# Kernel tuning notes

Hardware: AMD Instinct MI355X
Metric: run time of the kernel (lower is better)

Reference implementation:

```python
import jax, jax.numpy as jnp
import numpy as np

B, T, V = 4, 2048, 2048
D = 256   # state_dim
R = 512   # inner_dim
EPS = float(jnp.finfo(jnp.float32).eps)  # F.rms_norm default eps = dtype eps


def rms_norm(x):
    return x * jax.lax.rsqrt(jnp.mean(x * x, axis=-1, keepdims=True) + EPS)


def setup_inputs() -> dict:
    key = jax.random.key(0)
    ks = jax.random.split(key, 9)
    std = 0.02
    return {
        "x": jax.random.normal(ks[0], (B, T, V), dtype=jnp.float32),
        "Wq": jax.random.normal(ks[1], (D, V), dtype=jnp.float32) * std,
        "Wk": jax.random.normal(ks[2], (D, V), dtype=jnp.float32) * std,
        "Wv": jax.random.normal(ks[3], (D, V), dtype=jnp.float32) * std,
        "Wo": jax.random.normal(ks[4], (V, D), dtype=jnp.float32) * std,
        "decay_logit": jnp.float32(3.0),
        "q_out_scale": jnp.float32(0.1),
        "Wdown": jax.random.normal(ks[5], (R, V), dtype=jnp.float32) * std,
        "Wup": jax.random.normal(ks[6], (V, R), dtype=jnp.float32) * std,
        "t_bias": jnp.zeros((R,), dtype=jnp.float32),
        "t_out_scale": jnp.float32(0.1),
        "q_scale": jnp.ones((1,), dtype=jnp.float32),
        "t_scale": jnp.ones((1,), dtype=jnp.float32),
    }


def qtable(x, Wq, Wk, Wv, Wo, decay_logit, out_scale):
    # x: (B,T,V)
    q = jnp.einsum('btv,dv->btd', x, Wq)
    k = jnp.einsum('btv,dv->btd', x, Wk)
    v = jnp.einsum('btv,dv->btd', x, Wv)
    scores = jnp.einsum('btd,bsd->bts', q, k)  # (B,T,T)
    decay = jax.nn.sigmoid(decay_logit)
    pos = jnp.arange(T)
    diff = pos[None, :] - pos[:, None]  # diff[t,s] = s - t ... matches torch (unsqueeze(0)-unsqueeze(1))
    causal = (diff > 0).astype(jnp.float32)
    weights = decay ** jnp.clip(diff.astype(jnp.float32) - 1.0, 0.0, None) * causal
    scores = scores * weights[None, :, :]
    retrieved = jnp.einsum('bts,bsd->btd', scores, v)
    return jnp.einsum('btd,vd->btv', retrieved, Wo) * out_scale


def transform(x, Wdown, Wup, bias, out_scale):
    h = jnp.einsum('btv,rv->btr', x, Wdown) + bias
    h = jax.nn.gelu(h, approximate=False)
    return jnp.einsum('btr,vr->btv', h, Wup) * out_scale


def reference(x, Wq, Wk, Wv, Wo, decay_logit, q_out_scale,
              Wdown, Wup, t_bias, t_out_scale, q_scale, t_scale):
    x = x + q_scale * qtable(rms_norm(x), Wq, Wk, Wv, Wo, decay_logit, q_out_scale)
    x = x + t_scale * transform(rms_norm(x), Wdown, Wup, t_bias, t_out_scale)
    return x
```

## Files before the change

kernel.cpp:

```cpp
#include <hip/hip_runtime.h>
#include <cmath>

typedef _Float16 f16;
typedef _Float16 f16x8 __attribute__((ext_vector_type(8)));
typedef _Float16 f16x4 __attribute__((ext_vector_type(4)));
typedef float f32x4 __attribute__((ext_vector_type(4)));

#define MFMA16(a, b, c) __builtin_amdgcn_mfma_f32_16x16x32_f16(a, b, c, 0, 0, 0)

static constexpr int Bsz = 4;
static constexpr int T = 2048;
static constexpr int V = 2048;
static constexpr int D = 256;
static constexpr int R = 512;
static constexpr int M = Bsz * T;

__device__ __forceinline__ void load_lds16(const f16* g, f16* l) {
    __builtin_amdgcn_global_load_lds(
        (const __attribute__((address_space(1))) unsigned int*)(unsigned long long)g,
        (__attribute__((address_space(3))) unsigned int*)(unsigned int)(unsigned long long)l,
        16, 0, 0);
}

__global__ __launch_bounds__(256) void conv_all(const float* __restrict__ s0,
                                                const float* __restrict__ s1,
                                                const float* __restrict__ s2,
                                                const float* __restrict__ s3,
                                                const float* __restrict__ s4,
                                                const float* __restrict__ s5,
                                                f16* __restrict__ dst) {
    int idx = (blockIdx.x * 256 + threadIdx.x) * 4;
    if (idx >= 4194304) return;
    const float* src; int off;
    if      (idx <  524288) { src = s0; off = idx; }
    else if (idx < 1048576) { src = s1; off = idx - 524288; }
    else if (idx < 1572864) { src = s2; off = idx - 1048576; }
    else if (idx < 2097152) { src = s3; off = idx - 1572864; }
    else if (idx < 3145728) { src = s4; off = idx - 2097152; }
    else                    { src = s5; off = idx - 3145728; }
    float4 v = *(const float4*)&src[off];
    f16x4 o;
    o[0] = (f16)v.x; o[1] = (f16)v.y; o[2] = (f16)v.z; o[3] = (f16)v.w;
    *(f16x4*)&dst[idx] = o;
}

__global__ __launch_bounds__(256) void rmsnorm_kernel(const float* __restrict__ x,
                                                      f16* __restrict__ out) {
    int row = blockIdx.x;
    const float* xr = x + (size_t)row * V;
    int tid = threadIdx.x;
    float4 v0 = ((const float4*)xr)[tid];
    float4 v1 = ((const float4*)xr)[tid + 256];
    float ss = v0.x * v0.x + v0.y * v0.y + v0.z * v0.z + v0.w * v0.w
             + v1.x * v1.x + v1.y * v1.y + v1.z * v1.z + v1.w * v1.w;
    #pragma unroll
    for (int o = 32; o > 0; o >>= 1) ss += __shfl_xor(ss, o);
    __shared__ float wsum[4];
    if ((tid & 63) == 0) wsum[tid >> 6] = ss;
    __syncthreads();
    float tot = wsum[0] + wsum[1] + wsum[2] + wsum[3];
    float s = rsqrtf(tot / (float)V + 1.1920929e-07f);
    f16* orow = out + (size_t)row * V;
    f16x4 o0, o1;
    o0[0] = (f16)(v0.x * s); o0[1] = (f16)(v0.y * s);
    o0[2] = (f16)(v0.z * s); o0[3] = (f16)(v0.w * s);
    o1[0] = (f16)(v1.x * s); o1[1] = (f16)(v1.y * s);
    o1[2] = (f16)(v1.z * s); o1[3] = (f16)(v1.w * s);
    *(f16x4*)&orow[tid * 4] = o0;
    *(f16x4*)&orow[1024 + tid * 4] = o1;
}

__global__ __launch_bounds__(256) void rmsnorm_f16(const f16* __restrict__ x,
                                                   f16* __restrict__ out) {
    int row = blockIdx.x;
    int tid = threadIdx.x;
    const f16* xr = x + (size_t)row * V;
    f16x8 v = *(const f16x8*)&xr[tid * 8];
    float f[8];
    float ss = 0.f;
    #pragma unroll
    for (int j = 0; j < 8; j++) { f[j] = (float)v[j]; ss += f[j] * f[j]; }
    #pragma unroll
    for (int o = 32; o > 0; o >>= 1) ss += __shfl_xor(ss, o);
    __shared__ float wsum[4];
    if ((tid & 63) == 0) wsum[tid >> 6] = ss;
    __syncthreads();
    float tot = wsum[0] + wsum[1] + wsum[2] + wsum[3];
    float s = rsqrtf(tot / (float)V + 1.1920929e-07f);
    f16x8 o;
    #pragma unroll
    for (int j = 0; j < 8; j++) o[j] = (f16)(f[j] * s);
    *(f16x8*)&out[(size_t)row * V + tid * 8] = o;
}

struct GemmEpi {
    const float* residf;
    const f16* residh;
    float* outf;
    f16* outh;
    f16* out_q; f16* out_k; f16* out_vT;
    f16* out_h;
    const float* bias;
    const float* sA; const float* sB;
};

template <int MODE>
__global__ __launch_bounds__(256) void gemm_nt(const f16* __restrict__ A,
                                               const f16* __restrict__ Bm,
                                               int K, GemmEpi e) {
    __shared__ f16 Asl[2][128 * 32];
    __shared__ f16 Bsl[2][128 * 32];
    int tid = threadIdx.x;
    int lane = tid & 63, wv = tid >> 6;
    int wm = wv >> 1, wn = wv & 1;
    int quad = lane >> 4, l16 = lane & 15;
    int m0 = blockIdx.x * 128, n0 = blockIdx.y * 128;
    f32x4 acc[4][4] = {};

    int srow = lane >> 2;
    int scg = (lane & 3) ^ ((lane >> 3) & 3);
    const f16* Ag0 = &A[(size_t)(m0 + 16 * wv + srow) * K + scg * 8];
    const f16* Ag1 = &A[(size_t)(m0 + 16 * (wv + 4) + srow) * K + scg * 8];
    const f16* Bg0 = &Bm[(size_t)(n0 + 16 * wv + srow) * K + scg * 8];
    const f16* Bg1 = &Bm[(size_t)(n0 + 16 * (wv + 4) + srow) * K + scg * 8];
    int lo0 = (16 * wv) * 32, lo1 = (16 * (wv + 4)) * 32;

    int fs = quad ^ ((l16 >> 1) & 3);
    int niter = K >> 5;

    load_lds16(Ag0, &Asl[0][lo0]);
    load_lds16(Ag1, &Asl[0][lo1]);
    load_lds16(Bg0, &Bsl[0][lo0]);
    load_lds16(Bg1, &Bsl[0][lo1]);

    for (int i = 0; i < niter; i++) {
        int cur = i & 1;
        __builtin_amdgcn_s_barrier();
        if (i + 1 < niter) {
            int k0 = (i + 1) << 5;
            int nb = cur ^ 1;
            load_lds16(Ag0 + k0, &Asl[nb][lo0]);
            load_lds16(Ag1 + k0, &Asl[nb][lo1]);
            load_lds16(Bg0 + k0, &Bsl[nb][lo0]);
            load_lds16(Bg1 + k0, &Bsl[nb][lo1]);
            asm volatile("s_waitcnt vmcnt(4)" ::: "memory");
        } else {
            asm volatile("s_waitcnt vmcnt(0)" ::: "memory");
        }
        __builtin_amdgcn_s_barrier();
        f16x8 af[4], bf[4];
        #pragma unroll
        for (int j = 0; j < 4; j++)
            af[j] = *(const f16x8*)&Asl[cur][(64 * wm + 16 * j + l16) * 32 + fs * 8];
        #pragma unroll
        for (int j = 0; j < 4; j++)
            bf[j] = *(const f16x8*)&Bsl[cur][(64 * wn + 16 * j + l16) * 32 + fs * 8];
        #pragma unroll
        for (int mi = 0; mi < 4; mi++)
            #pragma unroll
            for (int ni = 0; ni < 4; ni++)
                acc[mi][ni] = MFMA16(af[mi], bf[ni], acc[mi][ni]);
    }

    float s = 0.f;
    if (MODE == 1 || MODE == 3) s = e.sA[0] * e.sB[0];
    #pragma unroll
    for (int mi = 0; mi < 4; mi++) {
        #pragma unroll
        for (int ni = 0; ni < 4; ni++) {
            int ml = 64 * wm + 16 * mi + quad * 4;
            int nl = 64 * wn + 16 * ni + l16;
            int gn = n0 + nl;
            #pragma unroll
            for (int i = 0; i < 4; i++) {
                int gm = m0 + ml + i;
                float vv = acc[mi][ni][i];
                if (MODE == 0) {
                    if (gn < 256) {
                        e.out_q[(size_t)gm * D + gn] = (f16)vv;
                    } else if (gn < 512) {
                        e.out_k[(size_t)gm * D + (gn - 256)] = (f16)vv;
                    } else {
                        int d = gn - 512;
                        int b = gm >> 11, t = gm & 2047;
                        e.out_vT[((size_t)b * D + d) * T + t] = (f16)vv;
                    }
                } else if (MODE == 1) {
                    size_t o = (size_t)gm * V + gn;
                    e.outh[o] = (f16)(e.residf[o] + s * vv);
                } else if (MODE == 2) {
                    float z = vv + e.bias[gn];
                    float g = 0.5f * z * (1.f + erff(z * 0.70710678118654752f));
                    e.out_h[(size_t)gm * R + gn] = (f16)g;
                } else {
                    size_t o = (size_t)gm * V + gn;
                    e.outf[o] = (float)e.residh[o] + s * vv;
                }
            }
        }
    }
}

__global__ __launch_bounds__(256) void attn_kernel(const f16* __restrict__ q,
                                                   const f16* __restrict__ k,
                                                   const f16* __restrict__ vT,
                                                   f16* __restrict__ ret,
                                                   const float* __restrict__ decay_logit) {
    __shared__ f16 Ksl[64 * 264];
    __shared__ f16 Psl[64 * 72];
    int tid = threadIdx.x, lane = tid & 63, wv = tid >> 6;
    int quad = lane >> 4, l16 = lane & 15;
    int b = blockIdx.y, t0 = blockIdx.x * 64;
    const f16* qb = q + (size_t)b * T * D;
    const f16* kb = k + (size_t)b * T * D;
    const f16* vb = vT + (size_t)b * D * T;
    f16* rb = ret + (size_t)b * T * D;

    float dl = decay_logit[0];
    float decay = 1.f / (1.f + expf(-dl));
    float l2d = log2f(decay);
    float nl2d = -l2d;

    int tq = t0 + 16 * wv + l16;
    f16x8 qf[8];
    #pragma unroll
    for (int kk = 0; kk < 8; kk++)
        qf[kk] = *(const f16x8*)&qb[(size_t)tq * D + kk * 32 + quad * 8];

    f32x4 acc2[4][4] = {};

    for (int s0 = t0; s0 < T; s0 += 64) {
        if ((float)(s0 - t0 - 64) * nl2d > 25.f) break;
        __syncthreads();
        #pragma unroll
        for (int p = 0; p < 8; p++) {
            int e0 = p * 2048 + tid * 8;
            int rr = e0 >> 8, cc = e0 & 255;
            *(f16x8*)&Ksl[rr * 264 + cc] = *(const f16x8*)&kb[(size_t)(s0 + rr) * D + cc];
        }
        __syncthreads();
        f32x4 sacc[4] = {};
        #pragma unroll
        for (int ni = 0; ni < 4; ni++) {
            #pragma unroll
            for (int kk = 0; kk < 8; kk++) {
                f16x8 bf = *(const f16x8*)&Ksl[(16 * ni + l16) * 264 + kk * 32 + quad * 8];
                sacc[ni] = MFMA16(qf[kk], bf, sacc[ni]);
            }
        }
        #pragma unroll
        for (int ni = 0; ni < 4; ni++) {
            int s_ = s0 + 16 * ni + l16;
            #pragma unroll
            for (int i = 0; i < 4; i++) {
                int t_ = t0 + 16 * wv + quad * 4 + i;
                int diff = s_ - t_;
                float w = (diff > 0) ? exp2f((float)(diff - 1) * l2d) : 0.f;
                Psl[(16 * wv + quad * 4 + i) * 72 + 16 * ni + l16] = (f16)(sacc[ni][i] * w);
            }
        }
        __syncthreads();
        #pragma unroll
        for (int kk = 0; kk < 2; kk++) {
            f16x8 pa[4], vf[4];
            #pragma unroll
            for (int mi = 0; mi < 4; mi++)
                pa[mi] = *(const f16x8*)&Psl[(16 * mi + l16) * 72 + kk * 32 + quad * 8];
            #pragma unroll
            for (int ni = 0; ni < 4; ni++)
                vf[ni] = *(const f16x8*)&vb[(size_t)(64 * wv + 16 * ni + l16) * T + s0 + kk * 32 + quad * 8];
            #pragma unroll
            for (int mi = 0; mi < 4; mi++)
                #pragma unroll
                for (int ni = 0; ni < 4; ni++)
                    acc2[mi][ni] = MFMA16(pa[mi], vf[ni], acc2[mi][ni]);
        }
    }

    #pragma unroll
    for (int mi = 0; mi < 4; mi++) {
        #pragma unroll
        for (int ni = 0; ni < 4; ni++) {
            int t_ = t0 + 16 * mi + quad * 4;
            int d_ = 64 * wv + 16 * ni + l16;
            #pragma unroll
            for (int i = 0; i < 4; i++)
                rb[(size_t)(t_ + i) * D + d_] = (f16)acc2[mi][ni][i];
        }
    }
}

extern "C" void kernel_launch(void* const* d_in, const int* in_sizes, int n_in,
                              void* d_out, int out_size, void* d_ws, size_t ws_size,
                              hipStream_t stream) {
    const float* x           = (const float*)d_in[0];
    const float* Wq          = (const float*)d_in[1];
    const float* Wk          = (const float*)d_in[2];
    const float* Wv          = (const float*)d_in[3];
    const float* Wo          = (const float*)d_in[4];
    const float* decay_logit = (const float*)d_in[5];
    const float* q_out_scale = (const float*)d_in[6];
    const float* Wdown       = (const float*)d_in[7];
    const float* Wup         = (const float*)d_in[8];
    const float* t_bias      = (const float*)d_in[9];
    const float* t_out_scale = (const float*)d_in[10];
    const float* q_scale     = (const float*)d_in[11];
    const float* t_scale     = (const float*)d_in[12];

    char* ws = (char*)d_ws;
    f16* Wqkv16  = (f16*)ws;  ws += (size_t)768 * V * 2;
    f16* Wo16    = (f16*)ws;  ws += (size_t)V * D * 2;
    f16* Wdown16 = (f16*)ws;  ws += (size_t)R * V * 2;
    f16* Wup16   = (f16*)ws;  ws += (size_t)V * R * 2;
    f16* xn16    = (f16*)ws;  ws += (size_t)M * V * 2;
    f16* q16     = (f16*)ws;  ws += (size_t)M * D * 2;
    f16* k16     = (f16*)ws;  ws += (size_t)M * D * 2;
    f16* vT16    = (f16*)ws;  ws += (size_t)Bsz * D * T * 2;
    f16* ret16   = (f16*)ws;  ws += (size_t)M * D * 2;
    f16* x2_16   = (f16*)ws;  ws += (size_t)M * V * 2;
    f16* h16     = q16;

    float* out = (float*)d_out;

    conv_all<<<dim3(4096), 256, 0, stream>>>(Wq, Wk, Wv, Wo, Wdown, Wup, Wqkv16);

    rmsnorm_kernel<<<dim3(M), 256, 0, stream>>>(x, xn16);

    {
        GemmEpi e = {};
        e.out_q = q16; e.out_k = k16; e.out_vT = vT16;
        gemm_nt<0><<<dim3(M / 128, 768 / 128), 256, 0, stream>>>(xn16, Wqkv16, V, e);
    }

    attn_kernel<<<dim3(T / 64, Bsz), 256, 0, stream>>>(q16, k16, vT16, ret16, decay_logit);

    {
        GemmEpi e = {};
        e.residf = x; e.outh = x2_16; e.sA = q_scale; e.sB = q_out_scale;
        gemm_nt<1><<<dim3(M / 128, V / 128), 256, 0, stream>>>(ret16, Wo16, D, e);
    }

    rmsnorm_f16<<<dim3(M), 256, 0, stream>>>(x2_16, xn16);

    {
        GemmEpi e = {};
        e.out_h = h16; e.bias = t_bias;
        gemm_nt<2><<<dim3(M / 128, R / 128), 256, 0, stream>>>(xn16, Wdown16, V, e);
    }

    {
        GemmEpi e = {};
        e.residh = x2_16; e.outf = out; e.sA = t_scale; e.sB = t_out_scale;
        gemm_nt<3><<<dim3(M / 128, V / 128), 256, 0, stream>>>(h16, Wup16, R, e);
    }
}
```

Baseline: 320.7 us.

## Add multi-stage LDS prefetch to GEMMs and restructure attention to 32-row tiles

The GEMM kernel gets a templated stage count: the long-K GEMMs (QKV and down projection) use a 4-deep global-to-LDS prefetch pipeline with vmcnt waits sized to the number of outstanding stages, while the short-K GEMMs keep double buffering. The attention kernel now processes 32 query rows per block instead of 64, doubling the grid. Each wave reads its own K rows directly from global memory, so the shared K tile and its copy are gone and one barrier is removed per step. This trades LDS staging and K reuse across waves for more parallelism and less LDS, with clamped indices at the sequence edge.

```diff
diff --git a/kernel.cpp b/kernel.cpp
--- a/kernel.cpp
+++ b/kernel.cpp
@@ -104,12 +104,12 @@
     const float* sA; const float* sB;
 };
 
-template <int MODE>
+template <int MODE, int STAGES>
 __global__ __launch_bounds__(256) void gemm_nt(const f16* __restrict__ A,
                                                const f16* __restrict__ Bm,
                                                int K, GemmEpi e) {
-    __shared__ f16 Asl[2][128 * 32];
-    __shared__ f16 Bsl[2][128 * 32];
+    __shared__ f16 Asl[STAGES][128 * 32];
+    __shared__ f16 Bsl[STAGES][128 * 32];
     int tid = threadIdx.x;
     int lane = tid & 63, wv = tid >> 6;
     int wm = wv >> 1, wn = wv & 1;
@@ -127,25 +127,41 @@
 
     int fs = quad ^ ((l16 >> 1) & 3);
     int niter = K >> 5;
-
-    load_lds16(Ag0, &Asl[0][lo0]);
-    load_lds16(Ag1, &Asl[0][lo1]);
-    load_lds16(Bg0, &Bsl[0][lo0]);
-    load_lds16(Bg1, &Bsl[0][lo1]);
+    constexpr int PF = STAGES - 1;
+
+    #pragma unroll
+    for (int t = 0; t < PF; ++t) {
+        if (t < niter) {
+            int k0 = t << 5;
+            load_lds16(Ag0 + k0, &Asl[t][lo0]);
+            load_lds16(Ag1 + k0, &Asl[t][lo1]);
+            load_lds16(Bg0 + k0, &Bsl[t][lo0]);
+            load_lds16(Bg1 + k0, &Bsl[t][lo1]);
+        }
+    }
 
     for (int i = 0; i < niter; i++) {
-        int cur = i & 1;
+        int cur = i & (STAGES - 1);
         __builtin_amdgcn_s_barrier();
-        if (i + 1 < niter) {
-            int k0 = (i + 1) << 5;
-            int nb = cur ^ 1;
+        int nt = i + PF;
+        if (nt < niter) {
+            int k0 = nt << 5;
+            int nb = nt & (STAGES - 1);
             load_lds16(Ag0 + k0, &Asl[nb][lo0]);
             load_lds16(Ag1 + k0, &Asl[nb][lo1]);
             load_lds16(Bg0 + k0, &Bsl[nb][lo0]);
             load_lds16(Bg1 + k0, &Bsl[nb][lo1]);
-            asm volatile("s_waitcnt vmcnt(4)" ::: "memory");
+        }
+        int ahead = niter - 1 - i;
+        if (ahead > PF) ahead = PF;
+        if constexpr (STAGES == 4) {
+            if (ahead == 3)      asm volatile("s_waitcnt vmcnt(12)" ::: "memory");
+            else if (ahead == 2) asm volatile("s_waitcnt vmcnt(8)" ::: "memory");
+            else if (ahead == 1) asm volatile("s_waitcnt vmcnt(4)" ::: "memory");
+            else                 asm volatile("s_waitcnt vmcnt(0)" ::: "memory");
         } else {
-            asm volatile("s_waitcnt vmcnt(0)" ::: "memory");
+            if (ahead >= 1)      asm volatile("s_waitcnt vmcnt(4)" ::: "memory");
+            else                 asm volatile("s_waitcnt vmcnt(0)" ::: "memory");
         }
         __builtin_amdgcn_s_barrier();
         f16x8 af[4], bf[4];
@@ -206,11 +222,10 @@
                                                    const f16* __restrict__ vT,
                                                    f16* __restrict__ ret,
                                                    const float* __restrict__ decay_logit) {
-    __shared__ f16 Ksl[64 * 264];
-    __shared__ f16 Psl[64 * 72];
+    __shared__ f16 Psl[32 * 72];
     int tid = threadIdx.x, lane = tid & 63, wv = tid >> 6;
     int quad = lane >> 4, l16 = lane & 15;
-    int b = blockIdx.y, t0 = blockIdx.x * 64;
+    int b = blockIdx.y, t0 = blockIdx.x * 32;
     const f16* qb = q + (size_t)b * T * D;
     const f16* kb = k + (size_t)b * T * D;
     const f16* vb = vT + (size_t)b * D * T;
@@ -221,56 +236,51 @@
     float l2d = log2f(decay);
     float nl2d = -l2d;
 
-    int tq = t0 + 16 * wv + l16;
-    f16x8 qf[8];
-    #pragma unroll
-    for (int kk = 0; kk < 8; kk++)
-        qf[kk] = *(const f16x8*)&qb[(size_t)tq * D + kk * 32 + quad * 8];
-
-    f32x4 acc2[4][4] = {};
+    f16x8 qf[2][8];
+    #pragma unroll
+    for (int mi = 0; mi < 2; mi++)
+        #pragma unroll
+        for (int kk = 0; kk < 8; kk++)
+            qf[mi][kk] = *(const f16x8*)&qb[(size_t)(t0 + 16 * mi + l16) * D + kk * 32 + quad * 8];
+
+    f32x4 acc2[2][4] = {};
 
     for (int s0 = t0; s0 < T; s0 += 64) {
-        if ((float)(s0 - t0 - 64) * nl2d > 25.f) break;
+        if ((float)(s0 - t0 - 32) * nl2d > 25.f) break;
+        int srow = s0 + 16 * wv + l16;
+        int srcl = srow < T ? srow : T - 1;
+        f32x4 sacc[2] = {};
+        #pragma unroll
+        for (int kk = 0; kk < 8; kk++) {
+            f16x8 bf = *(const f16x8*)&kb[(size_t)srcl * D + kk * 32 + quad * 8];
+            sacc[0] = MFMA16(qf[0][kk], bf, sacc[0]);
+            sacc[1] = MFMA16(qf[1][kk], bf, sacc[1]);
+        }
         __syncthreads();
         #pragma unroll
-        for (int p = 0; p < 8; p++) {
-            int e0 = p * 2048 + tid * 8;
-            int rr = e0 >> 8, cc = e0 & 255;
-            *(f16x8*)&Ksl[rr * 264 + cc] = *(const f16x8*)&kb[(size_t)(s0 + rr) * D + cc];
+        for (int mi = 0; mi < 2; mi++) {
+            #pragma unroll
+            for (int i = 0; i < 4; i++) {
+                int t_ = t0 + 16 * mi + quad * 4 + i;
+                int diff = srow - t_;
+                float w = (diff > 0 && srow < T) ? exp2f((float)(diff - 1) * l2d) : 0.f;
+                Psl[(16 * mi + quad * 4 + i) * 72 + 16 * wv + l16] = (f16)(sacc[mi][i] * w);
+            }
         }
         __syncthreads();
-        f32x4 sacc[4] = {};
-        #pragma unroll
-        for (int ni = 0; ni < 4; ni++) {
-            #pragma unroll
-            for (int kk = 0; kk < 8; kk++) {
-                f16x8 bf = *(const f16x8*)&Ksl[(16 * ni + l16) * 264 + kk * 32 + quad * 8];
-                sacc[ni] = MFMA16(qf[kk], bf, sacc[ni]);
-            }
-        }
-        #pragma unroll
-        for (int ni = 0; ni < 4; ni++) {
-            int s_ = s0 + 16 * ni + l16;
-            #pragma unroll
-            for (int i = 0; i < 4; i++) {
-                int t_ = t0 + 16 * wv + quad * 4 + i;
-                int diff = s_ - t_;
-                float w = (diff > 0) ? exp2f((float)(diff - 1) * l2d) : 0.f;
-                Psl[(16 * wv + quad * 4 + i) * 72 + 16 * ni + l16] = (f16)(sacc[ni][i] * w);
-            }
-        }
-        __syncthreads();
         #pragma unroll
         for (int kk = 0; kk < 2; kk++) {
-            f16x8 pa[4], vf[4];
-            #pragma unroll
-            for (int mi = 0; mi < 4; mi++)
+            int sb = s0 + kk * 32 + quad * 8;
+            if (sb >= T) sb = T - 8;
+            f16x8 pa[2], vf[4];
+            #pragma unroll
+            for (int mi = 0; mi < 2; mi++)
                 pa[mi] = *(const f16x8*)&Psl[(16 * mi + l16) * 72 + kk * 32 + quad * 8];
             #pragma unroll
             for (int ni = 0; ni < 4; ni++)
-                vf[ni] = *(const f16x8*)&vb[(size_t)(64 * wv + 16 * ni + l16) * T + s0 + kk * 32 + quad * 8];
-            #pragma unroll
-            for (int mi = 0; mi < 4; mi++)
+                vf[ni] = *(const f16x8*)&vb[(size_t)(64 * wv + 16 * ni + l16) * T + sb];
+            #pragma unroll
+            for (int mi = 0; mi < 2; mi++)
                 #pragma unroll
                 for (int ni = 0; ni < 4; ni++)
                     acc2[mi][ni] = MFMA16(pa[mi], vf[ni], acc2[mi][ni]);
@@ -278,7 +288,7 @@
     }
 
     #pragma unroll
-    for (int mi = 0; mi < 4; mi++) {
+    for (int mi = 0; mi < 2; mi++) {
         #pragma unroll
         for (int ni = 0; ni < 4; ni++) {
             int t_ = t0 + 16 * mi + quad * 4;
@@ -329,15 +339,15 @@
     {
         GemmEpi e = {};
         e.out_q = q16; e.out_k = k16; e.out_vT = vT16;
-        gemm_nt<0><<<dim3(M / 128, 768 / 128), 256, 0, stream>>>(xn16, Wqkv16, V, e);
-    }
-
-    attn_kernel<<<dim3(T / 64, Bsz), 256, 0, stream>>>(q16, k16, vT16, ret16, decay_logit);
+        gemm_nt<0, 4><<<dim3(M / 128, 768 / 128), 256, 0, stream>>>(xn16, Wqkv16, V, e);
+    }
+
+    attn_kernel<<<dim3(T / 32, Bsz), 256, 0, stream>>>(q16, k16, vT16, ret16, decay_logit);
 
     {
         GemmEpi e = {};
         e.residf = x; e.outh = x2_16; e.sA = q_scale; e.sB = q_out_scale;
-        gemm_nt<1><<<dim3(M / 128, V / 128), 256, 0, stream>>>(ret16, Wo16, D, e);
+        gemm_nt<1, 2><<<dim3(M / 128, V / 128), 256, 0, stream>>>(ret16, Wo16, D, e);
     }
 
     rmsnorm_f16<<<dim3(M), 256, 0, stream>>>(x2_16, xn16);
@@ -345,12 +355,12 @@
     {
         GemmEpi e = {};
         e.out_h = h16; e.bias = t_bias;
-        gemm_nt<2><<<dim3(M / 128, R / 128), 256, 0, stream>>>(xn16, Wdown16, V, e);
+        gemm_nt<2, 4><<<dim3(M / 128, R / 128), 256, 0, stream>>>(xn16, Wdown16, V, e);
     }
 
     {
         GemmEpi e = {};
         e.residh = x2_16; e.outf = out; e.sA = t_scale; e.sB = t_out_scale;
-        gemm_nt<3><<<dim3(M / 128, V / 128), 256, 0, stream>>>(h16, Wup16, R, e);
-    }
-}
+        gemm_nt<3, 2><<<dim3(M / 128, V / 128), 256, 0, stream>>>(h16, Wup16, R, e);
+    }
+}
```

Measured after the change: 313.2 us. -2.3%, faster.
